# Optimization experiments

Measured on AMD Instinct MI355X. Metric: run time of the kernel, lower is better.

Reference implementation:

```python
import jax, jax.numpy as jnp
import numpy as np

N, E, G = 100000, 1000000, 128   # nodes, edges, graphs
EMB, H, L, T = 128, 64, 3, 2     # embed dim, hidden, n conv layers, target classes
BN_EPS = 1e-5


def setup_inputs() -> dict:
    key = jax.random.key(0)
    ks = iter(jax.random.split(key, 64))

    def nrm(shape, s=0.1):
        return jax.random.normal(next(ks), shape, jnp.float32) * s

    def pos(shape):  # positive running variances
        return jax.random.uniform(next(ks), shape, jnp.float32, 0.5, 1.5)

    node_ids = jax.random.randint(next(ks), (N,), 0, N)
    edge_index = jax.random.randint(next(ks), (2, E), 0, N)
    batch = jnp.sort(jax.random.randint(next(ks), (N,), 0, G))
    emb_table = nrm((N, EMB)).at[0].set(0.0)  # padding_idx=0

    inp = dict(node_ids=node_ids, edge_index=edge_index, batch=batch,
               emb_table=emb_table,
               fh_W1=nrm((EMB, H)), fh_b1=nrm((H,)),
               fh_g1=1.0 + nrm((H,)), fh_bt1=nrm((H,)), fh_m1=nrm((H,)), fh_v1=pos((H,)),
               fh_W2=nrm((H, H)), fh_b2=nrm((H,)),
               fh_g2=1.0 + nrm((H,)), fh_bt2=nrm((H,)), fh_m2=nrm((H,)), fh_v2=pos((H,)),
               conv_W1=nrm((L, H, H)), conv_b1=nrm((L, H)),
               conv_g1=1.0 + nrm((L, H)), conv_bt1=nrm((L, H)), conv_m1=nrm((L, H)), conv_v1=pos((L, H)),
               conv_W2=nrm((L, H, H)), conv_b2=nrm((L, H)),
               conv_g2=1.0 + nrm((L, H)), conv_bt2=nrm((L, H)), conv_m2=nrm((L, H)), conv_v2=pos((L, H)),
               lin_W=nrm((L + 1, H, T)), lin_b=nrm((L + 1, T)))
    return inp


def _bn(x, g, b, m, v):
    # inference-mode BatchNorm1d with running stats
    return (x - m) * (g / jnp.sqrt(v + BN_EPS)) + b


def _mlp(x, W1, b1, g1, bt1, m1, v1, W2, b2, g2, bt2, m2, v2):
    h = jax.nn.relu(_bn(x @ W1 + b1, g1, bt1, m1, v1))
    return jax.nn.relu(_bn(h @ W2 + b2, g2, bt2, m2, v2))


def reference(node_ids, edge_index, batch, emb_table,
              fh_W1, fh_b1, fh_g1, fh_bt1, fh_m1, fh_v1,
              fh_W2, fh_b2, fh_g2, fh_bt2, fh_m2, fh_v2,
              conv_W1, conv_b1, conv_g1, conv_bt1, conv_m1, conv_v1,
              conv_W2, conv_b2, conv_g2, conv_bt2, conv_m2, conv_v2,
              lin_W, lin_b):
    src, dst = edge_index[0], edge_index[1]
    x = emb_table[node_ids]                                   # [N, EMB]
    x = _mlp(x, fh_W1, fh_b1, fh_g1, fh_bt1, fh_m1, fh_v1,
             fh_W2, fh_b2, fh_g2, fh_bt2, fh_m2, fh_v2)       # [N, H]
    # layer 0 readout: linear -> sum-pool (dropout p=0)
    out = jax.ops.segment_sum(x @ lin_W[0] + lin_b[0], batch, num_segments=G)
    for l in range(L):
        # GINConv with eps=0: MLP(x + scatter_add of neighbor feats)
        agg = jax.ops.segment_sum(x[src], dst, num_segments=N)  # [N, H]
        x = _mlp(x + agg,
                 conv_W1[l], conv_b1[l], conv_g1[l], conv_bt1[l], conv_m1[l], conv_v1[l],
                 conv_W2[l], conv_b2[l], conv_g2[l], conv_bt2[l], conv_m2[l], conv_v2[l])
        pooled = jax.ops.segment_sum(x, batch, num_segments=G)  # [G, H]
        out = out + pooled @ lin_W[l + 1] + lin_b[l + 1]
    return jax.nn.softmax(out, axis=-1)                        # [G, T]
```

## Files before the change

### kernel.cpp

```cpp
#include <hip/hip_runtime.h>
#include <hip/hip_bf16.h>

#define NN 100000
#define EE 1000000
#define GG 128
#define NT 782
#define BN_EPS 1e-5f
#define SLOTS 48

#define X0_OFF    0L
#define X1_OFF    3250000L
#define COL2_OFF  6500000L
#define WT1_OFF   12806144L
#define C1_OFF    12814336L
#define WT2_OFF   12814400L
#define C2_OFF    12818496L
#define WTC1_OFF  12818560L
#define CC1_OFF   12830848L
#define WTC2_OFF  12831040L
#define CC2_OFF   12843328L
#define POOL_OFF  12843520L
#define CNT_OFF   12876288L
#define CUR_OFF   13876416L
#define OVFC_OFF  13976416L
#define OVF_OFF   13976420L

#define OVF_CAP 4096

__device__ __forceinline__ float bf_lo(unsigned v) { return __uint_as_float(v << 16); }
__device__ __forceinline__ float bf_hi(unsigned v) { return __uint_as_float(v & 0xffff0000u); }
__device__ __forceinline__ unsigned f2bf(float f) {
    unsigned b = __float_as_uint(f);
    return (b + 0x7fffu + ((b >> 16) & 1u)) >> 16;
}

__global__ void prep_kernel(
    const float* __restrict__ fh_W1, const float* __restrict__ fh_b1, const float* __restrict__ fh_g1,
    const float* __restrict__ fh_bt1, const float* __restrict__ fh_m1, const float* __restrict__ fh_v1,
    const float* __restrict__ fh_W2, const float* __restrict__ fh_b2, const float* __restrict__ fh_g2,
    const float* __restrict__ fh_bt2, const float* __restrict__ fh_m2, const float* __restrict__ fh_v2,
    const float* __restrict__ cW1, const float* __restrict__ cb1, const float* __restrict__ cg1,
    const float* __restrict__ cbt1, const float* __restrict__ cm1, const float* __restrict__ cv1,
    const float* __restrict__ cW2, const float* __restrict__ cb2, const float* __restrict__ cg2,
    const float* __restrict__ cbt2, const float* __restrict__ cm2, const float* __restrict__ cv2,
    float* __restrict__ ws)
{
    int job = blockIdx.x;
    const float *W, *b, *g, *bt, *m, *v;
    float *Wo, *Co;
    int K;
    if (job == 0) {
        W = fh_W1; b = fh_b1; g = fh_g1; bt = fh_bt1; m = fh_m1; v = fh_v1;
        Wo = ws + WT1_OFF; Co = ws + C1_OFF; K = 128;
    } else if (job == 1) {
        W = fh_W2; b = fh_b2; g = fh_g2; bt = fh_bt2; m = fh_m2; v = fh_v2;
        Wo = ws + WT2_OFF; Co = ws + C2_OFF; K = 64;
    } else if (job <= 4) {
        int l = job - 2;
        W = cW1 + l * 4096; b = cb1 + l * 64; g = cg1 + l * 64; bt = cbt1 + l * 64;
        m = cm1 + l * 64; v = cv1 + l * 64;
        Wo = ws + WTC1_OFF + l * 4096; Co = ws + CC1_OFF + l * 64; K = 64;
    } else {
        int l = job - 5;
        W = cW2 + l * 4096; b = cb2 + l * 64; g = cg2 + l * 64; bt = cbt2 + l * 64;
        m = cm2 + l * 64; v = cv2 + l * 64;
        Wo = ws + WTC2_OFF + l * 4096; Co = ws + CC2_OFF + l * 64; K = 64;
    }
    int tot = 64 * K;
    for (int i = threadIdx.x; i < tot; i += blockDim.x) {
        int j = i & 63;
        float s = g[j] * rsqrtf(v[j] + BN_EPS);
        Wo[i] = W[i] * s;
    }
    if (threadIdx.x < 64) {
        int j = threadIdx.x;
        float s = g[j] * rsqrtf(v[j] + BN_EPS);
        Co[j] = (b[j] - m[j]) * s + bt[j];
    }
}

__global__ __launch_bounds__(256) void fill2_kernel(
    const int* __restrict__ edges, int* __restrict__ cursor, int* __restrict__ col2,
    int* __restrict__ ovfCnt, int* __restrict__ ovf)
{
    int e = blockIdx.x * blockDim.x + threadIdx.x;
    if (e >= EE) return;
    int dst = edges[EE + e];
    int src = edges[e];
    int p = atomicAdd(&cursor[dst], 1);
    if (p < SLOTS) {
        col2[(long)dst * SLOTS + p] = src;
    } else {
        int q = atomicAdd(ovfCnt, 1);
        if (q < OVF_CAP) { ovf[2 * q] = dst; ovf[2 * q + 1] = src; }
    }
}

__global__ __launch_bounds__(256) void gconv_fused_kernel(
    const unsigned* __restrict__ xin, const int* __restrict__ cursor, const int* __restrict__ col2,
    const int* __restrict__ ovfCnt, const int* __restrict__ ovf,
    const float* __restrict__ W1s, const float* __restrict__ C1v,
    const float* __restrict__ W2s, const float* __restrict__ C2v,
    const int* __restrict__ batch,
    unsigned* __restrict__ xout, float* __restrict__ pooled)
{
    __shared__ float ldsB[64 * 65];
    __shared__ int sh_no;
    int t = threadIdx.x;
    int lane = t & 63;
    int wv = t >> 6;
    int nbase = blockIdx.x << 6;
    if (t == 0) sh_no = *ovfCnt;

    int nL = nbase + lane;
    int myDeg = 0;
    if (nL < NN) {
        myDeg = cursor[nL];
        if (myDeg > SLOTS) myDeg = SLOTS;
    }

    {
        int q = lane >> 3, c = lane & 7;
        const uint4* x4 = (const uint4*)xin;
        for (int s = 0; s < 16; s++) {
            int i = (wv << 4) + s;
            int n = nbase + i;
            if (n < NN) {
                int deg = __shfl(myDeg, i);
                long cb = (long)n * SLOTS;
                float acc[8];
                if (q == 0) {
                    uint4 u = x4[(long)n * 8 + c];
                    acc[0] = bf_lo(u.x); acc[1] = bf_hi(u.x);
                    acc[2] = bf_lo(u.y); acc[3] = bf_hi(u.y);
                    acc[4] = bf_lo(u.z); acc[5] = bf_hi(u.z);
                    acc[6] = bf_lo(u.w); acc[7] = bf_hi(u.w);
                } else {
#pragma unroll
                    for (int r = 0; r < 8; r++) acc[r] = 0.f;
                }
                for (int b2 = q; b2 < deg; b2 += 8) {
                    int sc = col2[cb + b2];
                    uint4 u = x4[(long)sc * 8 + c];
                    acc[0] += bf_lo(u.x); acc[1] += bf_hi(u.x);
                    acc[2] += bf_lo(u.y); acc[3] += bf_hi(u.y);
                    acc[4] += bf_lo(u.z); acc[5] += bf_hi(u.z);
                    acc[6] += bf_lo(u.w); acc[7] += bf_hi(u.w);
                }
#pragma unroll
                for (int d = 8; d <= 32; d <<= 1) {
#pragma unroll
                    for (int r = 0; r < 8; r++) acc[r] += __shfl_xor(acc[r], d);
                }
                if (q == 0) {
                    int f = c << 3;
#pragma unroll
                    for (int r = 0; r < 8; r++) ldsB[(f + r) * 65 + i] = acc[r];
                }
            }
        }
    }
    __syncthreads();

    if (sh_no > 0) {
        if (t == 0) {
            int no = sh_no; if (no > OVF_CAP) no = OVF_CAP;
            for (int i = 0; i < no; i++) {
                int dst = ovf[2 * i];
                if (dst >= nbase && dst < nbase + 64 && dst < NN) {
                    int src = ovf[2 * i + 1];
                    int loc = dst - nbase;
                    const unsigned* xr = xin + ((long)src << 5);
                    for (int f = 0; f < 32; f++) {
                        unsigned v = xr[f];
                        ldsB[(2 * f) * 65 + loc] += bf_lo(v);
                        ldsB[(2 * f + 1) * 65 + loc] += bf_hi(v);
                    }
                }
            }
        }
        __syncthreads();
    }

    int wvu = __builtin_amdgcn_readfirstlane(wv);
    float a[16];
#pragma unroll
    for (int j = 0; j < 16; j++) a[j] = C1v[wvu * 16 + j];
#pragma unroll 4
    for (int k = 0; k < 64; k++) {
        float xk = ldsB[k * 65 + lane];
        const float* w = W1s + k * 64 + wvu * 16;
#pragma unroll
        for (int j = 0; j < 16; j++) a[j] += xk * w[j];
    }
    __syncthreads();
#pragma unroll
    for (int j = 0; j < 16; j++) ldsB[(wvu * 16 + j) * 65 + lane] = fmaxf(a[j], 0.f);
    __syncthreads();

    float o[16];
#pragma unroll
    for (int j = 0; j < 16; j++) o[j] = C2v[wvu * 16 + j];
#pragma unroll 4
    for (int k = 0; k < 64; k++) {
        float hk = ldsB[k * 65 + lane];
        const float* w = W2s + k * 64 + wvu * 16;
#pragma unroll
        for (int j = 0; j < 16; j++) o[j] += hk * w[j];
    }
#pragma unroll
    for (int j = 0; j < 16; j++) o[j] = fmaxf(o[j], 0.f);

    int n = nbase + lane;
    if (n < NN) {
        unsigned u[8];
#pragma unroll
        for (int p = 0; p < 8; p++) u[p] = f2bf(o[2 * p]) | (f2bf(o[2 * p + 1]) << 16);
        uint4* xo = (uint4*)(xout + ((long)n << 5) + (wvu << 3));
        xo[0] = make_uint4(u[0], u[1], u[2], u[3]);
        xo[1] = make_uint4(u[4], u[5], u[6], u[7]);
    }

    int bg = (n < NN) ? batch[n] : -1;
    int bprev = __shfl(bg, (lane == 0) ? 0 : lane - 1);
    bool bound = (lane == 0) || (bg != bprev);
    unsigned long long m = __ballot(bound);
    int p = 0;
    while (p < 64) {
        unsigned long long rest = (p < 63) ? (m & (~0ULL << (p + 1))) : 0ULL;
        int np = rest ? (__ffsll((long long)rest) - 1) : 64;
        int g = __shfl(bg, p);
        if (g >= 0) {
            bool in = (lane >= p) && (lane < np);
#pragma unroll
            for (int j = 0; j < 16; j++) {
                float v = in ? o[j] : 0.f;
                v += __shfl_xor(v, 1);  v += __shfl_xor(v, 2);
                v += __shfl_xor(v, 4);  v += __shfl_xor(v, 8);
                v += __shfl_xor(v, 16); v += __shfl_xor(v, 32);
                if (lane == p) unsafeAtomicAdd(&pooled[g * 64 + wvu * 16 + j], v);
            }
        }
        p = np;
    }
}

__global__ __launch_bounds__(256) void embed_fused_kernel(
    const int* __restrict__ node_ids, const float* __restrict__ emb,
    const float* __restrict__ W1s, const float* __restrict__ C1v,
    const float* __restrict__ W2s, const float* __restrict__ C2v,
    const int* __restrict__ batch,
    unsigned* __restrict__ xb, float* __restrict__ pooled, float* __restrict__ cnt)
{
    __shared__ float ldsB[64 * 129];
    __shared__ int sh_nid[64];
    int t = threadIdx.x;
    int lane = t & 63;
    int wvu = __builtin_amdgcn_readfirstlane(t >> 6);
    int nbase = blockIdx.x << 6;
    if (t < 64) {
        int n0 = nbase + t;
        sh_nid[t] = (n0 < NN) ? node_ids[n0] : 0;
    }
    __syncthreads();
    for (int idx = t; idx < 8192; idx += 256) {
        int r = idx >> 7, c = idx & 127;
        ldsB[r * 129 + c] = emb[(long)sh_nid[r] * 128 + c];
    }
    __syncthreads();
    float a[16];
#pragma unroll
    for (int j = 0; j < 16; j++) a[j] = C1v[wvu * 16 + j];
#pragma unroll 4
    for (int k = 0; k < 128; k++) {
        float ek = ldsB[lane * 129 + k];
        const float* w = W1s + k * 64 + wvu * 16;
#pragma unroll
        for (int j = 0; j < 16; j++) a[j] += ek * w[j];
    }
    __syncthreads();
#pragma unroll
    for (int j = 0; j < 16; j++) ldsB[(wvu * 16 + j) * 65 + lane] = fmaxf(a[j], 0.f);
    __syncthreads();
    float o[16];
#pragma unroll
    for (int j = 0; j < 16; j++) o[j] = C2v[wvu * 16 + j];
#pragma unroll 4
    for (int k = 0; k < 64; k++) {
        float hk = ldsB[k * 65 + lane];
        const float* w = W2s + k * 64 + wvu * 16;
#pragma unroll
        for (int j = 0; j < 16; j++) o[j] += hk * w[j];
    }
#pragma unroll
    for (int j = 0; j < 16; j++) o[j] = fmaxf(o[j], 0.f);

    int n = nbase + lane;
    if (n < NN) {
        unsigned u[8];
#pragma unroll
        for (int p = 0; p < 8; p++) u[p] = f2bf(o[2 * p]) | (f2bf(o[2 * p + 1]) << 16);
        uint4* xo = (uint4*)(xb + ((long)n << 5) + (wvu << 3));
        xo[0] = make_uint4(u[0], u[1], u[2], u[3]);
        xo[1] = make_uint4(u[4], u[5], u[6], u[7]);
    }

    int bg = (n < NN) ? batch[n] : -1;
    int bprev = __shfl(bg, (lane == 0) ? 0 : lane - 1);
    bool bound = (lane == 0) || (bg != bprev);
    unsigned long long m = __ballot(bound);
    int p = 0;
    while (p < 64) {
        unsigned long long rest = (p < 63) ? (m & (~0ULL << (p + 1))) : 0ULL;
        int np = rest ? (__ffsll((long long)rest) - 1) : 64;
        int g = __shfl(bg, p);
        if (g >= 0) {
            bool in = (lane >= p) && (lane < np);
#pragma unroll
            for (int j = 0; j < 16; j++) {
                float v = in ? o[j] : 0.f;
                v += __shfl_xor(v, 1);  v += __shfl_xor(v, 2);
                v += __shfl_xor(v, 4);  v += __shfl_xor(v, 8);
                v += __shfl_xor(v, 16); v += __shfl_xor(v, 32);
                if (lane == p) unsafeAtomicAdd(&pooled[g * 64 + wvu * 16 + j], v);
            }
            if (wvu == 0 && lane == p) unsafeAtomicAdd(&cnt[g], (float)(np - p));
        }
        p = np;
    }
}

__global__ void final_kernel(
    const float* __restrict__ pooled, const float* __restrict__ cnt,
    const float* __restrict__ linW, const float* __restrict__ linb,
    float* __restrict__ outp)
{
    int g = threadIdx.x;
    if (g >= GG) return;
    float z0 = 0.f, z1 = 0.f;
    float c = cnt[g];
    for (int l = 0; l < 4; l++) {
        const float* p = pooled + (long)l * GG * 64 + (long)g * 64;
        const float* W = linW + l * 128;
        float bscale = (l == 0) ? c : 1.f;
        float s0 = linb[l * 2 + 0] * bscale;
        float s1 = linb[l * 2 + 1] * bscale;
        for (int k = 0; k < 64; k++) {
            float pk = p[k];
            s0 += pk * W[k * 2 + 0];
            s1 += pk * W[k * 2 + 1];
        }
        z0 += s0; z1 += s1;
    }
    float mx = fmaxf(z0, z1);
    float e0 = expf(z0 - mx), e1 = expf(z1 - mx);
    float inv = 1.f / (e0 + e1);
    outp[g * 2 + 0] = e0 * inv;
    outp[g * 2 + 1] = e1 * inv;
}

extern "C" void kernel_launch(void* const* d_in, const int* in_sizes, int n_in,
                              void* d_out, int out_size, void* d_ws, size_t ws_size,
                              hipStream_t stream) {
    const int*   node_ids = (const int*)d_in[0];
    const int*   edges    = (const int*)d_in[1];
    const int*   batch    = (const int*)d_in[2];
    const float* emb      = (const float*)d_in[3];
    const float* fh_W1 = (const float*)d_in[4];
    const float* fh_b1 = (const float*)d_in[5];
    const float* fh_g1 = (const float*)d_in[6];
    const float* fh_bt1 = (const float*)d_in[7];
    const float* fh_m1 = (const float*)d_in[8];
    const float* fh_v1 = (const float*)d_in[9];
    const float* fh_W2 = (const float*)d_in[10];
    const float* fh_b2 = (const float*)d_in[11];
    const float* fh_g2 = (const float*)d_in[12];
    const float* fh_bt2 = (const float*)d_in[13];
    const float* fh_m2 = (const float*)d_in[14];
    const float* fh_v2 = (const float*)d_in[15];
    const float* cW1 = (const float*)d_in[16];
    const float* cb1 = (const float*)d_in[17];
    const float* cg1 = (const float*)d_in[18];
    const float* cbt1 = (const float*)d_in[19];
    const float* cm1 = (const float*)d_in[20];
    const float* cv1 = (const float*)d_in[21];
    const float* cW2 = (const float*)d_in[22];
    const float* cb2 = (const float*)d_in[23];
    const float* cg2 = (const float*)d_in[24];
    const float* cbt2 = (const float*)d_in[25];
    const float* cm2 = (const float*)d_in[26];
    const float* cv2 = (const float*)d_in[27];
    const float* linW = (const float*)d_in[28];
    const float* linb = (const float*)d_in[29];

    float*    ws     = (float*)d_ws;
    int*      cursor = (int*)(ws + CUR_OFF);
    int*      col2   = (int*)(ws + COL2_OFF);
    int*      ovfCnt = (int*)(ws + OVFC_OFF);
    int*      ovf    = (int*)(ws + OVF_OFF);
    unsigned* x0     = (unsigned*)(ws + X0_OFF);
    unsigned* x1     = (unsigned*)(ws + X1_OFF);

    prep_kernel<<<8, 256, 0, stream>>>(
        fh_W1, fh_b1, fh_g1, fh_bt1, fh_m1, fh_v1,
        fh_W2, fh_b2, fh_g2, fh_bt2, fh_m2, fh_v2,
        cW1, cb1, cg1, cbt1, cm1, cv1,
        cW2, cb2, cg2, cbt2, cm2, cv2, ws);

    hipMemsetAsync(ws + POOL_OFF, 0, (4L * GG * 64 + GG) * sizeof(float), stream);
    hipMemsetAsync(cursor, 0, (NN + 1) * sizeof(int) + (CUR_OFF + NN + 1 == OVFC_OFF + 1 ? 0 : 0), stream);
    hipMemsetAsync(ovfCnt, 0, sizeof(int), stream);

    fill2_kernel<<<(EE + 255) / 256, 256, 0, stream>>>(edges, cursor, col2, ovfCnt, ovf);

    const int FBLK = NT * 2;

    embed_fused_kernel<<<FBLK, 256, 0, stream>>>(
        node_ids, emb, ws + WT1_OFF, ws + C1_OFF, ws + WT2_OFF, ws + C2_OFF,
        batch, x0, ws + POOL_OFF, ws + CNT_OFF);

    unsigned* xin = x0;
    unsigned* xout = x1;
    for (int l = 0; l < 3; l++) {
        gconv_fused_kernel<<<FBLK, 256, 0, stream>>>(
            xin, cursor, col2, ovfCnt, ovf,
            ws + WTC1_OFF + l * 4096, ws + CC1_OFF + l * 64,
            ws + WTC2_OFF + l * 4096, ws + CC2_OFF + l * 64,
            batch, xout, ws + POOL_OFF + (long)(l + 1) * GG * 64);
        unsigned* tmp = xin; xin = xout; xout = tmp;
    }

    final_kernel<<<1, 128, 0, stream>>>(
        ws + POOL_OFF, ws + CNT_OFF, linW, linb, (float*)d_out);
}
```

Before: 491.2 us.

## Fuse edge bucketing with embedding MLP and fold memsets into prep kernel

The three buffer memsets are replaced by extra blocks in the weight-prep kernel that zero the cursor array (which also covers the overflow counter) and the pooled and count buffers. The edge-bucketing kernel and the embedding MLP kernel are merged into one launch: the first blocks do edge insertion and the rest do the embedding path, so the two independent stages can overlap on the GPU. The embedding gather now loads its 128-wide rows in two 64-column halves, which halves the shared-memory tile and may allow more resident blocks. The aim is fewer launches and memsets and better overlap, at the cost of mixing blocks with very different register and shared-memory needs in one launch.

```diff
diff --git a/kernel.cpp b/kernel.cpp
--- a/kernel.cpp
+++ b/kernel.cpp
@@ -7,6 +7,7 @@
 #define NT 782
 #define BN_EPS 1e-5f
 #define SLOTS 48
+#define NFILL ((EE + 255) / 256)
 
 #define X0_OFF    0L
 #define X1_OFF    3250000L
@@ -26,6 +27,8 @@
 #define OVF_OFF   13976420L
 
 #define OVF_CAP 4096
+#define ZERO_INTS (NN + 1 + 4 * GG * 64 + GG)
+#define ZBLK ((ZERO_INTS + 255) / 256)
 
 __device__ __forceinline__ float bf_lo(unsigned v) { return __uint_as_float(v << 16); }
 __device__ __forceinline__ float bf_hi(unsigned v) { return __uint_as_float(v & 0xffff0000u); }
@@ -46,6 +49,16 @@
     float* __restrict__ ws)
 {
     int job = blockIdx.x;
+    if (job >= 8) {
+        long idx = (long)(job - 8) * 256 + threadIdx.x;
+        if (idx < NN + 1) {
+            ((int*)(ws + CUR_OFF))[idx] = 0;
+        } else {
+            long i2 = idx - (NN + 1);
+            if (i2 < 4L * GG * 64 + GG) (ws + POOL_OFF)[i2] = 0.f;
+        }
+        return;
+    }
     const float *W, *b, *g, *bt, *m, *v;
     float *Wo, *Co;
     int K;
@@ -79,20 +92,113 @@
     }
 }
 
-__global__ __launch_bounds__(256) void fill2_kernel(
+__global__ __launch_bounds__(256) void prologue_kernel(
     const int* __restrict__ edges, int* __restrict__ cursor, int* __restrict__ col2,
-    int* __restrict__ ovfCnt, int* __restrict__ ovf)
+    int* __restrict__ ovfCnt, int* __restrict__ ovf,
+    const int* __restrict__ node_ids, const float* __restrict__ emb,
+    const float* __restrict__ W1s, const float* __restrict__ C1v,
+    const float* __restrict__ W2s, const float* __restrict__ C2v,
+    const int* __restrict__ batch,
+    unsigned* __restrict__ xb, float* __restrict__ pooled, float* __restrict__ cnt)
 {
-    int e = blockIdx.x * blockDim.x + threadIdx.x;
-    if (e >= EE) return;
-    int dst = edges[EE + e];
-    int src = edges[e];
-    int p = atomicAdd(&cursor[dst], 1);
-    if (p < SLOTS) {
-        col2[(long)dst * SLOTS + p] = src;
-    } else {
-        int q = atomicAdd(ovfCnt, 1);
-        if (q < OVF_CAP) { ovf[2 * q] = dst; ovf[2 * q + 1] = src; }
+    __shared__ float ldsB[64 * 65];
+    __shared__ int sh_nid[64];
+    int t = threadIdx.x;
+
+    if (blockIdx.x < NFILL) {
+        int e = blockIdx.x * 256 + t;
+        if (e < EE) {
+            int dst = edges[EE + e];
+            int src = edges[e];
+            int p = atomicAdd(&cursor[dst], 1);
+            if (p < SLOTS) {
+                col2[(long)dst * SLOTS + p] = src;
+            } else {
+                int q = atomicAdd(ovfCnt, 1);
+                if (q < OVF_CAP) { ovf[2 * q] = dst; ovf[2 * q + 1] = src; }
+            }
+        }
+        return;
+    }
+
+    int lane = t & 63;
+    int wvu = __builtin_amdgcn_readfirstlane(t >> 6);
+    int nbase = (int)(blockIdx.x - NFILL) << 6;
+    if (t < 64) {
+        int n0 = nbase + t;
+        sh_nid[t] = (n0 < NN) ? node_ids[n0] : 0;
+    }
+    __syncthreads();
+
+    float a[16];
+#pragma unroll
+    for (int j = 0; j < 16; j++) a[j] = C1v[wvu * 16 + j];
+
+#pragma unroll
+    for (int half = 0; half < 2; half++) {
+        for (int idx = t; idx < 4096; idx += 256) {
+            int r = idx >> 6, c = idx & 63;
+            ldsB[r * 65 + c] = emb[(long)sh_nid[r] * 128 + half * 64 + c];
+        }
+        __syncthreads();
+#pragma unroll 4
+        for (int k = 0; k < 64; k++) {
+            float ek = ldsB[lane * 65 + k];
+            const float* w = W1s + (half * 64 + k) * 64 + wvu * 16;
+#pragma unroll
+            for (int j = 0; j < 16; j++) a[j] += ek * w[j];
+        }
+        __syncthreads();
+    }
+
+#pragma unroll
+    for (int j = 0; j < 16; j++) ldsB[(wvu * 16 + j) * 65 + lane] = fmaxf(a[j], 0.f);
+    __syncthreads();
+    float o[16];
+#pragma unroll
+    for (int j = 0; j < 16; j++) o[j] = C2v[wvu * 16 + j];
+#pragma unroll 4
+    for (int k = 0; k < 64; k++) {
+        float hk = ldsB[k * 65 + lane];
+        const float* w = W2s + k * 64 + wvu * 16;
+#pragma unroll
+        for (int j = 0; j < 16; j++) o[j] += hk * w[j];
+    }
+#pragma unroll
+    for (int j = 0; j < 16; j++) o[j] = fmaxf(o[j], 0.f);
+
+    int n = nbase + lane;
+    if (n < NN) {
+        unsigned u[8];
+#pragma unroll
+        for (int p = 0; p < 8; p++) u[p] = f2bf(o[2 * p]) | (f2bf(o[2 * p + 1]) << 16);
+        uint4* xo = (uint4*)(xb + ((long)n << 5) + (wvu << 3));
+        xo[0] = make_uint4(u[0], u[1], u[2], u[3]);
+        xo[1] = make_uint4(u[4], u[5], u[6], u[7]);
+    }
+
+    int bg = (n < NN) ? batch[n] : -1;
+    int bprev = __shfl(bg, (lane == 0) ? 0 : lane - 1);
+    bool bound = (lane == 0) || (bg != bprev);
+    unsigned long long m = __ballot(bound);
+    int p = 0;
+    while (p < 64) {
+        unsigned long long rest = (p < 63) ? (m & (~0ULL << (p + 1))) : 0ULL;
+        int np = rest ? (__ffsll((long long)rest) - 1) : 64;
+        int g = __shfl(bg, p);
+        if (g >= 0) {
+            bool in = (lane >= p) && (lane < np);
+#pragma unroll
+            for (int j = 0; j < 16; j++) {
+                float v = in ? o[j] : 0.f;
+                v += __shfl_xor(v, 1);  v += __shfl_xor(v, 2);
+                v += __shfl_xor(v, 4);  v += __shfl_xor(v, 8);
+                v += __shfl_xor(v, 16); v += __shfl_xor(v, 32);
+                if (lane == p) unsafeAtomicAdd(&pooled[g * 64 + wvu * 16 + j], v);
+            }
+            if (wvu == 0 && lane == p) unsafeAtomicAdd(&cnt[g], (float)(np - p));
+        }
+        p = np;
     }
 }
 
@@ -240,91 +346,6 @@
                 v += __shfl_xor(v, 16); v += __shfl_xor(v, 32);
                 if (lane == p) unsafeAtomicAdd(&pooled[g * 64 + wvu * 16 + j], v);
             }
-        }
-        p = np;
-    }
-}
-
-__global__ __launch_bounds__(256) void embed_fused_kernel(
-    const int* __restrict__ node_ids, const float* __restrict__ emb,
-    const float* __restrict__ W1s, const float* __restrict__ C1v,
-    const float* __restrict__ W2s, const float* __restrict__ C2v,
-    const int* __restrict__ batch,
-    unsigned* __restrict__ xb, float* __restrict__ pooled, float* __restrict__ cnt)
-{
-    __shared__ float ldsB[64 * 129];
-    __shared__ int sh_nid[64];
-    int t = threadIdx.x;
-    int lane = t & 63;
-    int wvu = __builtin_amdgcn_readfirstlane(t >> 6);
-    int nbase = blockIdx.x << 6;
-    if (t < 64) {
-        int n0 = nbase + t;
-        sh_nid[t] = (n0 < NN) ? node_ids[n0] : 0;
-    }
-    __syncthreads();
-    for (int idx = t; idx < 8192; idx += 256) {
-        int r = idx >> 7, c = idx & 127;
-        ldsB[r * 129 + c] = emb[(long)sh_nid[r] * 128 + c];
-    }
-    __syncthreads();
-    float a[16];
-#pragma unroll
-    for (int j = 0; j < 16; j++) a[j] = C1v[wvu * 16 + j];
-#pragma unroll 4
-    for (int k = 0; k < 128; k++) {
-        float ek = ldsB[lane * 129 + k];
-        const float* w = W1s + k * 64 + wvu * 16;
-#pragma unroll
-        for (int j = 0; j < 16; j++) a[j] += ek * w[j];
-    }
-    __syncthreads();
-#pragma unroll
-    for (int j = 0; j < 16; j++) ldsB[(wvu * 16 + j) * 65 + lane] = fmaxf(a[j], 0.f);
-    __syncthreads();
-    float o[16];
-#pragma unroll
-    for (int j = 0; j < 16; j++) o[j] = C2v[wvu * 16 + j];
-#pragma unroll 4
-    for (int k = 0; k < 64; k++) {
-        float hk = ldsB[k * 65 + lane];
-        const float* w = W2s + k * 64 + wvu * 16;
-#pragma unroll
-        for (int j = 0; j < 16; j++) o[j] += hk * w[j];
-    }
-#pragma unroll
-    for (int j = 0; j < 16; j++) o[j] = fmaxf(o[j], 0.f);
-
-    int n = nbase + lane;
-    if (n < NN) {
-        unsigned u[8];
-#pragma unroll
-        for (int p = 0; p < 8; p++) u[p] = f2bf(o[2 * p]) | (f2bf(o[2 * p + 1]) << 16);
-        uint4* xo = (uint4*)(xb + ((long)n << 5) + (wvu << 3));
-        xo[0] = make_uint4(u[0], u[1], u[2], u[3]);
-        xo[1] = make_uint4(u[4], u[5], u[6], u[7]);
-    }
-
-    int bg = (n < NN) ? batch[n] : -1;
-    int bprev = __shfl(bg, (lane == 0) ? 0 : lane - 1);
-    bool bound = (lane == 0) || (bg != bprev);
-    unsigned long long m = __ballot(bound);
-    int p = 0;
-    while (p < 64) {
-        unsigned long long rest = (p < 63) ? (m & (~0ULL << (p + 1))) : 0ULL;
-        int np = rest ? (__ffsll((long long)rest) - 1) : 64;
-        int g = __shfl(bg, p);
-        if (g >= 0) {
-            bool in = (lane >= p) && (lane < np);
-#pragma unroll
-            for (int j = 0; j < 16; j++) {
-                float v = in ? o[j] : 0.f;
-                v += __shfl_xor(v, 1);  v += __shfl_xor(v, 2);
-                v += __shfl_xor(v, 4);  v += __shfl_xor(v, 8);
-                v += __shfl_xor(v, 16); v += __shfl_xor(v, 32);
-                if (lane == p) unsafeAtomicAdd(&pooled[g * 64 + wvu * 16 + j], v);
-            }
-            if (wvu == 0 && lane == p) unsafeAtomicAdd(&cnt[g], (float)(np - p));
         }
         p = np;
     }
@@ -401,21 +422,16 @@
     unsigned* x0     = (unsigned*)(ws + X0_OFF);
     unsigned* x1     = (unsigned*)(ws + X1_OFF);
 
-    prep_kernel<<<8, 256, 0, stream>>>(
+    prep_kernel<<<8 + ZBLK, 256, 0, stream>>>(
         fh_W1, fh_b1, fh_g1, fh_bt1, fh_m1, fh_v1,
         fh_W2, fh_b2, fh_g2, fh_bt2, fh_m2, fh_v2,
         cW1, cb1, cg1, cbt1, cm1, cv1,
         cW2, cb2, cg2, cbt2, cm2, cv2, ws);
 
-    hipMemsetAsync(ws + POOL_OFF, 0, (4L * GG * 64 + GG) * sizeof(float), stream);
-    hipMemsetAsync(cursor, 0, (NN + 1) * sizeof(int) + (CUR_OFF + NN + 1 == OVFC_OFF + 1 ? 0 : 0), stream);
-    hipMemsetAsync(ovfCnt, 0, sizeof(int), stream);
-
-    fill2_kernel<<<(EE + 255) / 256, 256, 0, stream>>>(edges, cursor, col2, ovfCnt, ovf);
-
     const int FBLK = NT * 2;
 
-    embed_fused_kernel<<<FBLK, 256, 0, stream>>>(
+    prologue_kernel<<<NFILL + FBLK, 256, 0, stream>>>(
+        edges, cursor, col2, ovfCnt, ovf,
         node_ids, emb, ws + WT1_OFF, ws + C1_OFF, ws + WT2_OFF, ws + C2_OFF,
         batch, x0, ws + POOL_OFF, ws + CNT_OFF);
 
```

Result: faster. 480.4 us (-2.2%).
